# Optimization experiments

Hardware: AMD Instinct MI355X
Metric: run time of the kernel (lower is better)

The kernel has to match this reference:

```python
import jax, jax.numpy as jnp
import numpy as np

V = 512          # vocab_size (= input_size = hidden_size of LSTMCell)
L = 128          # formula_max_len
PAD_ID = 0
SOS_ID = 1


def setup_inputs() -> dict:
    key = jax.random.key(0)
    k1, k2, k3, k4, k5 = jax.random.split(key, 5)
    B = 512
    s = 1.0 / np.sqrt(V)  # torch LSTMCell init scale
    return {
        "x": jax.random.normal(k1, (B, V), dtype=jnp.float32),
        "W_ih": jax.random.uniform(k2, (4 * V, V), jnp.float32, -s, s),
        "W_hh": jax.random.uniform(k3, (4 * V, V), jnp.float32, -s, s),
        "b_ih": jax.random.uniform(k4, (4 * V,), jnp.float32, -s, s),
        "b_hh": jax.random.uniform(k5, (4 * V,), jnp.float32, -s, s),
    }


def _decode(x, W_ih, W_hh, b_ih, b_hh):
    B = x.shape[0]
    dt = x.dtype
    sos = jax.nn.one_hot(SOS_ID, V, dtype=dt)
    pad = jax.nn.one_hot(PAD_ID, V, dtype=dt)

    h0 = x                      # hidden_state = x.squeeze()
    c0 = jnp.zeros_like(x)
    inp0 = jnp.broadcast_to(sos, (B, V))

    def step(carry, _):
        h, c, inp = carry
        # torch LSTMCell: gates = x W_ih^T + b_ih + h W_hh^T + b_hh, order i,f,g,o
        gates = inp @ W_ih.T + b_ih + h @ W_hh.T + b_hh   # [B, 4V]
        i, f, g, o = jnp.split(gates, 4, axis=-1)
        c_new = jax.nn.sigmoid(f) * c + jax.nn.sigmoid(i) * jnp.tanh(g)
        h_new = jax.nn.sigmoid(o) * jnp.tanh(c_new)
        probas = jax.nn.softmax(h_new, axis=-1)           # [B, V]
        nxt = jax.nn.one_hot(jnp.argmax(probas, axis=-1), V, dtype=dt)
        return (h_new, c_new, nxt), probas

    _, probas_seq = jax.lax.scan(step, (h0, c0, inp0), None, length=L - 1)
    # probas_seq: [L-1, B, V] -> [B, L-1, V]; last position stays PAD one-hot
    preds = jnp.swapaxes(probas_seq, 0, 1)
    pad_row = jnp.broadcast_to(pad, (B, 1, V))
    return jnp.concatenate([preds, pad_row], axis=1)      # [B, L, V]


def reference(x, W_ih, W_hh, b_ih, b_hh):
    return _decode(x, W_ih, W_hh, b_ih, b_hh)
```

## Files before the change

### kernel.cpp

```cpp
#include <hip/hip_runtime.h>

#define VSZ 512
#define LSEQ 128
#define NTHR 512
#define NBLK 256
#define NGRP 8
#define GBLK 32
#define SPIN_MAX (1u << 20)

using short8  = __attribute__((ext_vector_type(8))) short;
using short4v = __attribute__((ext_vector_type(4))) short;
using floatx4 = __attribute__((ext_vector_type(4))) float;
using ull2v   = __attribute__((ext_vector_type(2))) unsigned long long;

static __device__ __forceinline__ short f2bf(float f) {
    union { float f; unsigned u; } v; v.f = f;
    unsigned u = v.u;
    unsigned r = (u + 0x7fffu + ((u >> 16) & 1u)) >> 16;
    return (short)r;
}
static __device__ __forceinline__ float bf2f(short s) {
    union { unsigned u; float f; } v; v.u = ((unsigned)(unsigned short)s) << 16;
    return v.f;
}
static __device__ __forceinline__ float fast_rcp(float x) { return __builtin_amdgcn_rcpf(x); }
static __device__ __forceinline__ float sigm(float x)   { return fast_rcp(1.0f + __expf(-x)); }
static __device__ __forceinline__ float tanh_f(float x) { return 1.0f - 2.0f * fast_rcp(__expf(2.0f * x) + 1.0f); }

template<bool F> static __device__ __forceinline__ void ldx4f(floatx4& d, const float* p) {
    if constexpr (F) asm volatile("global_load_dwordx4 %0, %1, off sc0"     : "=v"(d) : "v"(p));
    else             asm volatile("global_load_dwordx4 %0, %1, off sc0 sc1" : "=v"(d) : "v"(p));
}
template<bool F> static __device__ __forceinline__ void ldx4u(ull2v& d, const unsigned long long* p) {
    if constexpr (F) asm volatile("global_load_dwordx4 %0, %1, off sc0"     : "=v"(d) : "v"(p));
    else             asm volatile("global_load_dwordx4 %0, %1, off sc0 sc1" : "=v"(d) : "v"(p));
}
template<bool F> static __device__ __forceinline__ void ldx4s(short8& d, const short* p) {
    if constexpr (F) asm volatile("global_load_dwordx4 %0, %1, off sc0"     : "=v"(d) : "v"(p));
    else             asm volatile("global_load_dwordx4 %0, %1, off sc0 sc1" : "=v"(d) : "v"(p));
}
template<bool F> static __device__ __forceinline__ void stg16(void* p, unsigned v) {
    if constexpr (F) asm volatile("global_store_short %0, %1, off sc0"     :: "v"(p), "v"(v) : "memory");
    else             asm volatile("global_store_short %0, %1, off sc0 sc1" :: "v"(p), "v"(v) : "memory");
}
template<bool F> static __device__ __forceinline__ void stg32(void* p, unsigned v) {
    if constexpr (F) asm volatile("global_store_dword %0, %1, off sc0"     :: "v"(p), "v"(v) : "memory");
    else             asm volatile("global_store_dword %0, %1, off sc0 sc1" :: "v"(p), "v"(v) : "memory");
}
template<bool F> static __device__ __forceinline__ void stg64(void* p, unsigned long long v) {
    if constexpr (F) asm volatile("global_store_dwordx2 %0, %1, off sc0"     :: "v"(p), "v"(v) : "memory");
    else             asm volatile("global_store_dwordx2 %0, %1, off sc0 sc1" :: "v"(p), "v"(v) : "memory");
}

static __device__ __forceinline__ unsigned atomic_add_dev(unsigned* p, unsigned v) {
    unsigned old;
    asm volatile("global_atomic_add %0, %1, %2, off sc0 sc1\n\ts_waitcnt vmcnt(0)"
                 : "=v"(old) : "v"(p), "v"(v) : "memory");
    return old;
}
static __device__ __forceinline__ unsigned ld_dev_u32(const unsigned* p) {
    unsigned v;
    asm volatile("global_load_dword %0, %1, off sc0 sc1\n\ts_waitcnt vmcnt(0)"
                 : "=v"(v) : "v"(p) : "memory");
    return v;
}

static __device__ __forceinline__ void group_barrier(unsigned* cnt, unsigned* gen,
                                                     int t, int tid) {
    asm volatile("s_waitcnt vmcnt(0)" ::: "memory");
    __builtin_amdgcn_s_barrier();
    if (tid == 0) {
        unsigned old = atomic_add_dev(cnt, 1u);
        if ((old & (GBLK - 1)) == (GBLK - 1)) atomic_add_dev(gen, 1u);
        unsigned it = 0;
        while (ld_dev_u32(gen) < (unsigned)(t + 1)) {
            if (++it > SPIN_MAX) break;
            __builtin_amdgcn_s_sleep(1);
        }
    }
    __builtin_amdgcn_s_barrier();
}

static __device__ __forceinline__ void grid_barrier_dev(unsigned* ctrl, int tid, int bid) {
    asm volatile("s_waitcnt vmcnt(0)" ::: "memory");
    __builtin_amdgcn_s_barrier();
    if (tid == 0) {
        unsigned* l1   = ctrl + 256 + (bid >> 4) * 32;
        unsigned* root = ctrl + 768;
        unsigned* gen  = ctrl + 800;
        unsigned old = atomic_add_dev(l1, 1u);
        if ((old & 15) == 15) {
            unsigned rold = atomic_add_dev(root, 1u);
            if ((rold & 15) == 15) atomic_add_dev(gen, 1u);
        }
        unsigned it = 0;
        while (ld_dev_u32(gen) < 1u) {
            if (++it > SPIN_MAX) break;
            __builtin_amdgcn_s_sleep(1);
        }
    }
    __builtin_amdgcn_s_barrier();
}

__global__ void prep_wb(const float* __restrict__ Whh, short* __restrict__ Wb) {
    int tid = threadIdx.x;
    int lane = tid & 63;
    int T = blockIdx.x * 8 + (tid >> 6);
    int g  = T & 3;
    int k  = (T >> 2) & 15;
    int vt = T >> 6;
    int l15 = lane & 15, lg = lane >> 4;
    const float* src = Whh + (size_t)(g * 512 + vt * 16 + l15) * 512 + k * 32 + lg * 8;
    short8 o;
#pragma unroll
    for (int i = 0; i < 8; ++i) o[i] = f2bf(src[i]);
    *(short8*)(Wb + (size_t)T * 512 + lane * 8) = o;
}

__global__ void prep_wxb(const float* __restrict__ Wih, const float* __restrict__ bih,
                         const float* __restrict__ bhh, short* __restrict__ Wxb) {
    __shared__ float tile[64][65];
    int j0 = blockIdx.x * 64;
    int a0 = blockIdx.y * 64;
    int tid = threadIdx.x;
    for (int i = tid; i < 4096; i += NTHR) {
        int r = i >> 6, c = i & 63;
        int jj = j0 + r;
        tile[r][c] = Wih[(size_t)jj * 512 + a0 + c] + bih[jj] + bhh[jj];
    }
    __syncthreads();
    int v0 = j0 & 511;
    for (int i = tid; i < 4096; i += NTHR) {
        int r = i >> 6, c = i & 63;
        Wxb[(((size_t)(a0 + r)) * 512 + v0 + c) * 4 + (j0 >> 9)] = f2bf(tile[c][r]);
    }
}

template<bool F>
static __device__ __forceinline__ void run_decoder(
    const float* __restrict__ x, const short* __restrict__ Wb, const short* __restrict__ Wxb,
    float* __restrict__ out,
    short* hbuf, float* psum, unsigned long long* pmax,
    unsigned* cnt, unsigned* gen,
    short (*hlds)[520], float (*gl)[4][17], float* rinvL, int* aidL,
    int tid, int g, int j) {

    const int lane = tid & 63;
    const int w    = tid >> 6;
    const int l15  = lane & 15;
    const int lg   = lane >> 4;
    const int v16  = tid & 15;
    const int rr   = tid >> 4;
    const int row0g = g * 64;
    const int jv   = j * 16 + v16;
    const int mt = w >> 1, g0 = (w & 1) * 2;

    short8 bb[16][2];
#pragma unroll
    for (int kc = 0; kc < 16; ++kc) {
        const short* p = Wb + ((size_t)j * 64 + kc * 4 + g0) * 512 + lane * 8;
        asm volatile("global_load_dwordx4 %0, %1, off"             : "=v"(bb[kc][0]) : "v"(p));
        asm volatile("global_load_dwordx4 %0, %1, off offset:1024" : "=v"(bb[kc][1]) : "v"(p));
    }
    asm volatile("s_waitcnt vmcnt(0)" ::: "memory");
    __builtin_amdgcn_sched_barrier(0);

    float cst[2] = {0.f, 0.f};
    float exv[2] = {0.f, 0.f};

    for (int t = 0; t < LSEQ - 1; ++t) {
        if (t == 0) {
            if (tid < 64) aidL[tid] = 1;
#pragma unroll
            for (int p = 0; p < 8; ++p) {
                int row = (tid >> 6) + 8 * p;
                const float* src = x + (size_t)(row0g + row) * VSZ + (tid & 63) * 8;
                short8 v;
#pragma unroll
                for (int e = 0; e < 8; ++e) v[e] = f2bf(src[e]);
                *(short8*)&hlds[row][(tid & 63) * 8] = v;
            }
        } else {
            const int tb = (t + 1) & 1;
            floatx4 s4v; ull2v m2a, m2b;
            const float* ps = psum + ((size_t)tb * 512 + row0g) * 32 + tid * 4;
            const unsigned long long* pm = pmax + ((size_t)tb * 512 + row0g) * 32 + tid * 4;
            ldx4f<F>(s4v, ps);
            ldx4u<F>(m2a, pm);
            ldx4u<F>(m2b, pm + 2);
            short8 stg[8];
            const short* hsrc = hbuf + (size_t)tb * (VSZ * VSZ);
#pragma unroll
            for (int p = 0; p < 8; ++p) {
                int row = (tid >> 6) + 8 * p;
                ldx4s<F>(stg[p], hsrc + (size_t)(row0g + row) * VSZ + (tid & 63) * 8);
            }
            asm volatile("s_waitcnt vmcnt(8)" ::: "memory");
            __builtin_amdgcn_sched_barrier(0);
            float s = (s4v[0] + s4v[1]) + (s4v[2] + s4v[3]);
            unsigned long long m = m2a[0] > m2a[1] ? m2a[0] : m2a[1];
            unsigned long long m2 = m2b[0] > m2b[1] ? m2b[0] : m2b[1];
            if (m2 > m) m = m2;
#pragma unroll
            for (int d = 1; d < 8; d <<= 1) {
                s += __shfl_xor(s, d);
                unsigned long long mo = __shfl_xor(m, d);
                if (mo > m) m = mo;
            }
            if ((tid & 7) == 0) {
                int r = tid >> 3;
                rinvL[r] = 1.0f / s;
                aidL[r]  = (int)(~(unsigned)m);
            }
            asm volatile("s_waitcnt vmcnt(0)" ::: "memory");
            __builtin_amdgcn_sched_barrier(0);
#pragma unroll
            for (int p = 0; p < 8; ++p) {
                int row = (tid >> 6) + 8 * p;
                *(short8*)&hlds[row][(tid & 63) * 8] = stg[p];
            }
        }
        __syncthreads();

        short4v wxv0, wxv1;
        {
            const short* gp0 = Wxb + ((size_t)aidL[rr]      * VSZ + jv) * 4;
            const short* gp1 = Wxb + ((size_t)aidL[rr + 32] * VSZ + jv) * 4;
            asm volatile("global_load_dwordx2 %0, %1, off" : "=v"(wxv0) : "v"(gp0));
            asm volatile("global_load_dwordx2 %0, %1, off" : "=v"(wxv1) : "v"(gp1));
        }

        if (t > 0) {
#pragma unroll
            for (int s2 = 0; s2 < 2; ++s2) {
                int r = rr + 32 * s2;
                __builtin_nontemporal_store(exv[s2] * rinvL[r],
                    &out[((size_t)(row0g + r) * LSEQ + (t - 1)) * VSZ + jv]);
            }
        }

        floatx4 a0v = {0,0,0,0}, a1v = {0,0,0,0};
#pragma unroll
        for (int kc = 0; kc < 16; ++kc) {
            short8 av = *(const short8*)&hlds[mt * 16 + l15][kc * 32 + lg * 8];
            a0v = __builtin_amdgcn_mfma_f32_16x16x32_bf16(av, bb[kc][0], a0v, 0, 0, 0);
            a1v = __builtin_amdgcn_mfma_f32_16x16x32_bf16(av, bb[kc][1], a1v, 0, 0, 0);
        }
#pragma unroll
        for (int q = 0; q < 4; ++q) {
            gl[mt * 16 + lg * 4 + q][g0][l15]     = a0v[q];
            gl[mt * 16 + lg * 4 + q][g0 + 1][l15] = a1v[q];
        }
        __syncthreads();

        asm volatile("s_waitcnt vmcnt(0)" ::: "memory");
        __builtin_amdgcn_sched_barrier(0);
#pragma unroll
        for (int s2 = 0; s2 < 2; ++s2) {
            int r = rr + 32 * s2;
            short4v wxv = s2 ? wxv1 : wxv0;
            float gi = gl[r][0][v16] + bf2f(wxv[0]);
            float gf = gl[r][1][v16] + bf2f(wxv[1]);
            float gg = gl[r][2][v16] + bf2f(wxv[2]);
            float go = gl[r][3][v16] + bf2f(wxv[3]);
            float cn = sigm(gf) * cst[s2] + sigm(gi) * tanh_f(gg);
            cst[s2] = cn;
            float hn = sigm(go) * tanh_f(cn);
            stg16<F>(hbuf + (size_t)(t & 1) * (VSZ * VSZ) + (size_t)(row0g + r) * VSZ + jv,
                     (unsigned)(unsigned short)f2bf(hn));
            float e = __expf(hn);
            exv[s2] = e;
            float s = e; float mv = e; int mi = jv;
#pragma unroll
            for (int m = 1; m < 16; m <<= 1) {
                s += __shfl_xor(s, m);
                float mv2 = __shfl_xor(mv, m);
                int   mi2 = __shfl_xor(mi, m);
                if (mv2 > mv || (mv2 == mv && mi2 < mi)) { mv = mv2; mi = mi2; }
            }
            if (v16 == 0) {
                size_t o32 = ((size_t)(t & 1) * 512 + row0g + r) * 32 + j;
                unsigned long long pk =
                    ((unsigned long long)__float_as_uint(mv) << 32) | (unsigned)(~(unsigned)mi);
                stg32<F>(psum + o32, __float_as_uint(s));
                stg64<F>(pmax + o32, pk);
            }
        }

        group_barrier(cnt, gen, t, tid);
    }

    {
        floatx4 s4v;
        ldx4f<F>(s4v, psum + (size_t)row0g * 32 + tid * 4);
        asm volatile("s_waitcnt vmcnt(0)" ::: "memory");
        __builtin_amdgcn_sched_barrier(0);
        float s = (s4v[0] + s4v[1]) + (s4v[2] + s4v[3]);
#pragma unroll
        for (int d = 1; d < 8; d <<= 1) s += __shfl_xor(s, d);
        if ((tid & 7) == 0) rinvL[tid >> 3] = 1.0f / s;
    }
    __syncthreads();
#pragma unroll
    for (int s2 = 0; s2 < 2; ++s2) {
        int r = rr + 32 * s2;
        __builtin_nontemporal_store(exv[s2] * rinvL[r],
            &out[((size_t)(row0g + r) * LSEQ + (LSEQ - 2)) * VSZ + jv]);
        __builtin_nontemporal_store((jv == 0) ? 1.0f : 0.0f,
            &out[((size_t)(row0g + r) * LSEQ + (LSEQ - 1)) * VSZ + jv]);
    }
}

__launch_bounds__(NTHR, 2)
__global__ void decoder_coop(const float* __restrict__ x, const short* __restrict__ Wb,
                             const short* __restrict__ Wxb,
                             short* hbuf_s, float* psum_s, unsigned long long* pmax_s,
                             short* hbuf_f, float* psum_f, unsigned long long* pmax_f,
                             unsigned* ctrl, float* __restrict__ out, int allow_fast) {
    __shared__ short hlds[64][520];
    __shared__ float gl[64][4][17];
    __shared__ float rinvL[64];
    __shared__ int   aidL[64];
    __shared__ int   sh_xcc, sh_slot, sh_ok;
    __shared__ unsigned sh_cnts[NGRP];

    const int tid = threadIdx.x;
    const int bid = blockIdx.x;

    if (tid == 0) {
        unsigned xcc;
        asm volatile("s_getreg_b32 %0, hwreg(HW_REG_XCC_ID)" : "=s"(xcc));
        xcc &= 7;
        unsigned slot = atomic_add_dev(ctrl + xcc * 32, 1u);
        sh_xcc = (int)xcc; sh_slot = (int)slot;
    }
    grid_barrier_dev(ctrl, tid, bid);
    if (tid < NGRP) sh_cnts[tid] = ld_dev_u32(ctrl + tid * 32);
    __syncthreads();
    if (tid == 0) {
        int ok = allow_fast && (sh_slot < GBLK);
#pragma unroll
        for (int g = 0; g < NGRP; ++g) ok = ok && (sh_cnts[g] == GBLK);
        sh_ok = ok;
    }
    __syncthreads();
    const int ok = sh_ok;
    const int g = ok ? sh_xcc : (bid & 7);
    const int j = ok ? sh_slot : (bid >> 3);

    if (ok)
        run_decoder<true >(x, Wb, Wxb, out, hbuf_f, psum_f, pmax_f,
                           ctrl + 1024 + g * 64, ctrl + 1024 + g * 64 + 32,
                           hlds, gl, rinvL, aidL, tid, g, j);
    else
        run_decoder<false>(x, Wb, Wxb, out, hbuf_s, psum_s, pmax_s,
                           ctrl + 1024 + g * 64, ctrl + 1024 + g * 64 + 32,
                           hlds, gl, rinvL, aidL, tid, g, j);
}

extern "C" void kernel_launch(void* const* d_in, const int* in_sizes, int n_in,
                              void* d_out, int out_size, void* d_ws, size_t ws_size,
                              hipStream_t stream) {
    const float* x    = (const float*)d_in[0];
    const float* W_ih = (const float*)d_in[1];
    const float* W_hh = (const float*)d_in[2];
    const float* b_ih = (const float*)d_in[3];
    const float* b_hh = (const float*)d_in[4];

    char* ws = (char*)d_ws;
    short* Wb     = (short*)ws;
    short* Wxb    = (short*)(ws + (2u << 20));
    short* hbuf_s = (short*)(ws + (4u << 20));
    float* psum_s = (float*)(ws + (5u << 20));
    unsigned long long* pmax_s = (unsigned long long*)(ws + (5u << 20) + (128u << 10));
    unsigned* ctrl = (unsigned*)(ws + (5u << 20) + (384u << 10));
    short* hbuf_f = (short*)(ws + (5u << 20) + (400u << 10));
    float* psum_f = (float*)(ws + (6u << 20) + (400u << 10));
    unsigned long long* pmax_f = (unsigned long long*)(ws + (6u << 20) + (528u << 10));
    const size_t needed = (6ull << 20) + (784ull << 10);
    int allow_fast = (ws_size >= needed) ? 1 : 0;

    prep_wb<<<256, NTHR, 0, stream>>>(W_hh, Wb);
    prep_wxb<<<dim3(32, 8), NTHR, 0, stream>>>(W_ih, b_ih, b_hh, Wxb);
    hipMemsetAsync(ctrl, 0, 16384, stream);

    float* outp = (float*)d_out;
    void* args[] = { (void*)&x, (void*)&Wb, (void*)&Wxb,
                     (void*)&hbuf_s, (void*)&psum_s, (void*)&pmax_s,
                     (void*)&hbuf_f, (void*)&psum_f, (void*)&pmax_f,
                     (void*)&ctrl, (void*)&outp, (void*)&allow_fast };
    hipLaunchCooperativeKernel((const void*)decoder_coop, dim3(NBLK), dim3(NTHR),
                               args, 0, stream);
}
```

Baseline: 625.4 us.

## Use split-phase tree barrier per group and overlap output stores with wait

Replaces the flat per-group counter barrier with a two-level tree: blocks first arrive on one of eight sub-counters, then the last arrival on each bumps a shared counter, which advances a generation word. The barrier is split into arrive and wait phases, and the previous step's normalized probability stores to the output are moved between them so they overlap with barrier latency. This aims to cut atomic contention on a single address and hide barrier wait time. In exchange it adds a chain of dependent atomics, a larger control-block layout per group, and a shorter spin timeout.

```diff
diff --git a/kernel.cpp b/kernel.cpp
--- a/kernel.cpp
+++ b/kernel.cpp
@@ -6,7 +6,8 @@
 #define NBLK 256
 #define NGRP 8
 #define GBLK 32
-#define SPIN_MAX (1u << 20)
+#define SPIN_MAX  (1u << 20)
+#define SPIN_STEP (1u << 16)
 
 using short8  = __attribute__((ext_vector_type(8))) short;
 using short4v = __attribute__((ext_vector_type(4))) short;
@@ -65,16 +66,22 @@
     return v;
 }
 
-static __device__ __forceinline__ void group_barrier(unsigned* cnt, unsigned* gen,
-                                                     int t, int tid) {
+static __device__ __forceinline__ void tree_arrive(unsigned* tb, int j, int tid) {
     asm volatile("s_waitcnt vmcnt(0)" ::: "memory");
     __builtin_amdgcn_s_barrier();
     if (tid == 0) {
-        unsigned old = atomic_add_dev(cnt, 1u);
-        if ((old & (GBLK - 1)) == (GBLK - 1)) atomic_add_dev(gen, 1u);
+        unsigned old = atomic_add_dev(tb + (j >> 2) * 32, 1u);
+        if ((old & 3) == 3) {
+            unsigned r = atomic_add_dev(tb + 256, 1u);
+            if ((r & 7) == 7) atomic_add_dev(tb + 288, 1u);
+        }
+    }
+}
+static __device__ __forceinline__ void tree_wait(unsigned* tb, int t, int tid) {
+    if (tid == 0) {
         unsigned it = 0;
-        while (ld_dev_u32(gen) < (unsigned)(t + 1)) {
-            if (++it > SPIN_MAX) break;
+        while (ld_dev_u32(tb + 288) < (unsigned)(t + 1)) {
+            if (++it > SPIN_STEP) break;
             __builtin_amdgcn_s_sleep(1);
         }
     }
@@ -140,8 +147,7 @@
 static __device__ __forceinline__ void run_decoder(
     const float* __restrict__ x, const short* __restrict__ Wb, const short* __restrict__ Wxb,
     float* __restrict__ out,
-    short* hbuf, float* psum, unsigned long long* pmax,
-    unsigned* cnt, unsigned* gen,
+    short* hbuf, float* psum, unsigned long long* pmax, unsigned* tb,
     short (*hlds)[520], float (*gl)[4][17], float* rinvL, int* aidL,
     int tid, int g, int j) {
 
@@ -181,15 +187,15 @@
                 *(short8*)&hlds[row][(tid & 63) * 8] = v;
             }
         } else {
-            const int tb = (t + 1) & 1;
+            const int tb2 = (t + 1) & 1;
             floatx4 s4v; ull2v m2a, m2b;
-            const float* ps = psum + ((size_t)tb * 512 + row0g) * 32 + tid * 4;
-            const unsigned long long* pm = pmax + ((size_t)tb * 512 + row0g) * 32 + tid * 4;
+            const float* ps = psum + ((size_t)tb2 * 512 + row0g) * 32 + tid * 4;
+            const unsigned long long* pm = pmax + ((size_t)tb2 * 512 + row0g) * 32 + tid * 4;
             ldx4f<F>(s4v, ps);
             ldx4u<F>(m2a, pm);
             ldx4u<F>(m2b, pm + 2);
             short8 stg[8];
-            const short* hsrc = hbuf + (size_t)tb * (VSZ * VSZ);
+            const short* hsrc = hbuf + (size_t)tb2 * (VSZ * VSZ);
 #pragma unroll
             for (int p = 0; p < 8; ++p) {
                 int row = (tid >> 6) + 8 * p;
@@ -230,15 +236,6 @@
             asm volatile("global_load_dwordx2 %0, %1, off" : "=v"(wxv1) : "v"(gp1));
         }
 
-        if (t > 0) {
-#pragma unroll
-            for (int s2 = 0; s2 < 2; ++s2) {
-                int r = rr + 32 * s2;
-                __builtin_nontemporal_store(exv[s2] * rinvL[r],
-                    &out[((size_t)(row0g + r) * LSEQ + (t - 1)) * VSZ + jv]);
-            }
-        }
-
         floatx4 a0v = {0,0,0,0}, a1v = {0,0,0,0};
 #pragma unroll
         for (int kc = 0; kc < 16; ++kc) {
@@ -255,6 +252,7 @@
 
         asm volatile("s_waitcnt vmcnt(0)" ::: "memory");
         __builtin_amdgcn_sched_barrier(0);
+        float pex0 = exv[0], pex1 = exv[1];
 #pragma unroll
         for (int s2 = 0; s2 < 2; ++s2) {
             int r = rr + 32 * s2;
@@ -287,7 +285,14 @@
             }
         }
 
-        group_barrier(cnt, gen, t, tid);
+        tree_arrive(tb, j, tid);
+        if (t > 0) {
+            __builtin_nontemporal_store(pex0 * rinvL[rr],
+                &out[((size_t)(row0g + rr) * LSEQ + (t - 1)) * VSZ + jv]);
+            __builtin_nontemporal_store(pex1 * rinvL[rr + 32],
+                &out[((size_t)(row0g + rr + 32) * LSEQ + (t - 1)) * VSZ + jv]);
+        }
+        tree_wait(tb, t, tid);
     }
 
     {
@@ -347,14 +352,13 @@
     const int ok = sh_ok;
     const int g = ok ? sh_xcc : (bid & 7);
     const int j = ok ? sh_slot : (bid >> 3);
+    unsigned* tb = ctrl + 1024 + g * 384;
 
     if (ok)
-        run_decoder<true >(x, Wb, Wxb, out, hbuf_f, psum_f, pmax_f,
-                           ctrl + 1024 + g * 64, ctrl + 1024 + g * 64 + 32,
+        run_decoder<true >(x, Wb, Wxb, out, hbuf_f, psum_f, pmax_f, tb,
                            hlds, gl, rinvL, aidL, tid, g, j);
     else
-        run_decoder<false>(x, Wb, Wxb, out, hbuf_s, psum_s, pmax_s,
-                           ctrl + 1024 + g * 64, ctrl + 1024 + g * 64 + 32,
+        run_decoder<false>(x, Wb, Wxb, out, hbuf_s, psum_s, pmax_s, tb,
                            hlds, gl, rinvL, aidL, tid, g, j);
 }
 
```

Measured after the change: 667.3 us. 6.7% more time.
